# Kernel optimization log

Hardware: AMD Instinct MI355X
Metric: run time of the kernel (lower is better)

The kernel has to match this reference:

```python
import jax, jax.numpy as jnp
import numpy as np

NOISE_EPS = 0.01
TOP_K = 2


def setup_inputs() -> dict:
    key = jax.random.key(0)
    k1, k2, k3, k4 = jax.random.split(key, 4)
    B, S, D, E = 8, 4096, 1024, 16
    x = jax.random.normal(k1, (B, S, D), dtype=jnp.float32)
    noise = jax.random.normal(k2, (B * S, E), dtype=jnp.float32)
    # xavier_uniform for Linear(D, E): bound = sqrt(6/(D+E))
    bound = float(np.sqrt(6.0 / (D + E)))
    W_gate = jax.random.uniform(k3, (E, D), dtype=jnp.float32, minval=-bound, maxval=bound)
    W_noise = jax.random.uniform(k4, (E, D), dtype=jnp.float32, minval=-bound, maxval=bound)
    return {"x": x, "noise": noise, "W_gate": W_gate, "W_noise": W_noise}


def reference(x, noise, W_gate, W_noise):
    # flatten tokens: (B,S,D) -> (N,D)
    orig_shape = x.shape
    x_flat = x.reshape(-1, x.shape[-1])
    clean_logits = jnp.einsum('nd,ed->ne', x_flat, W_gate)          # (N, E)
    noise_logits = jnp.einsum('nd,ed->ne', x_flat, W_noise)         # (N, E)
    noisy_logits = clean_logits + noise * jax.nn.softplus(noise_logits) * NOISE_EPS
    gates = jax.nn.softmax(noisy_logits, axis=-1)                   # (N, E)
    top_k_gates, top_k_indices = jax.lax.top_k(gates, TOP_K)        # (N, k)
    top_k_gates = top_k_gates / (jnp.sum(top_k_gates, axis=-1, keepdims=True) + 1e-8)
    load = jnp.sum(gates, axis=0)                                    # (E,)
    new_shape = orig_shape[:-1] + (TOP_K,)
    top_k_gates = top_k_gates.reshape(new_shape)
    top_k_indices = top_k_indices.reshape(new_shape)
    return top_k_gates, top_k_indices, load
```

## Files before the change

kernel.cpp:

```cpp
#include <hip/hip_runtime.h>
#include <hip/hip_bf16.h>
#include <math.h>

#define N_TOK 32768
#define DDIM 1024
#define NEXP 16
#define THREADS 256
#define TOK_PER_WAVE 16
#define TOK_PER_BLK 64
#define NBLK (N_TOK / TOK_PER_BLK)
#define KSTEPS (DDIM / 32)

typedef __attribute__((ext_vector_type(8))) short bf16x8;
typedef __attribute__((ext_vector_type(4))) float f32x4;

__device__ inline short f2bf(float f) {
    unsigned u = __builtin_bit_cast(unsigned, f);
    u += 0x7fffu + ((u >> 16) & 1u);
    return (short)(u >> 16);
}

__global__ __launch_bounds__(256) void make_wfrag(
    const float* __restrict__ Wg, const float* __restrict__ Wn,
    unsigned short* __restrict__ Wfrag)
{
    const int i    = blockIdx.x * 256 + threadIdx.x;
    const int j    = i & 7;
    const int lane = (i >> 3) & 63;
    const int tile = (i >> 9) & 1;
    const int s    = i >> 10;
    const int k    = s * 32 + (lane >> 4) * 8 + j;
    const float* W = tile ? Wn : Wg;
    Wfrag[i] = (unsigned short)f2bf(W[(size_t)(lane & 15) * DDIM + k]);
}

__global__ __launch_bounds__(THREADS) void router_mfma(
    const float* __restrict__ x, const float* __restrict__ noise,
    const unsigned short* __restrict__ Wfrag,
    float* __restrict__ out_gates, float* __restrict__ out_idx,
    float* __restrict__ partials)
{
    __shared__ float blk_load[NEXP];
    const int tid  = threadIdx.x;
    const int lane = tid & 63;
    const int w    = tid >> 6;
    if (tid < NEXP) blk_load[tid] = 0.0f;
    __syncthreads();

    const int tok = blockIdx.x * TOK_PER_BLK + w * TOK_PER_WAVE + (lane & 15);
    const int grp = lane >> 4;

    const float*          xb = x + (size_t)tok * DDIM + grp * 8;
    const unsigned short* wb = Wfrag + (size_t)lane * 8;

    f32x4 acc0 = {0.f, 0.f, 0.f, 0.f};
    f32x4 acc1 = {0.f, 0.f, 0.f, 0.f};

#pragma unroll 4
    for (int s = 0; s < KSTEPS; ++s) {
        const float4 lo = *(const float4*)(xb + s * 32);
        const float4 hi = *(const float4*)(xb + s * 32 + 4);
        const bf16x8 a0 = *(const bf16x8*)(wb + (size_t)(s * 2 + 0) * 512);
        const bf16x8 a1 = *(const bf16x8*)(wb + (size_t)(s * 2 + 1) * 512);
        bf16x8 b;
        b[0] = f2bf(lo.x); b[1] = f2bf(lo.y); b[2] = f2bf(lo.z); b[3] = f2bf(lo.w);
        b[4] = f2bf(hi.x); b[5] = f2bf(hi.y); b[6] = f2bf(hi.z); b[7] = f2bf(hi.w);
        acc0 = __builtin_amdgcn_mfma_f32_16x16x32_bf16(a0, b, acc0, 0, 0, 0);
        acc1 = __builtin_amdgcn_mfma_f32_16x16x32_bf16(a1, b, acc1, 0, 0, 0);
    }

    const float4 nz4 = *(const float4*)(noise + (size_t)tok * NEXP + grp * 4);
    const float nzv[4] = {nz4.x, nz4.y, nz4.z, nz4.w};

    float lg[4];
#pragma unroll
    for (int r = 0; r < 4; ++r) {
        const float cl = acc0[r];
        const float nl = acc1[r];
        const float sp = fmaxf(nl, 0.0f) + log1pf(expf(-fabsf(nl)));
        lg[r] = cl + nzv[r] * sp * 0.01f;
    }

    float m = fmaxf(fmaxf(lg[0], lg[1]), fmaxf(lg[2], lg[3]));
    m = fmaxf(m, __shfl_xor(m, 16, 64));
    m = fmaxf(m, __shfl_xor(m, 32, 64));

    float p[4];
    float ssum = 0.0f;
#pragma unroll
    for (int r = 0; r < 4; ++r) { p[r] = expf(lg[r] - m); ssum += p[r]; }
    ssum += __shfl_xor(ssum, 16, 64);
    ssum += __shfl_xor(ssum, 32, 64);
    const float inv = 1.0f / ssum;

    float g[4];
#pragma unroll
    for (int r = 0; r < 4; ++r) g[r] = p[r] * inv;

    float v1 = -1.0f, v2 = -1.0f;
    int   i1 = 0,     i2 = 0;
#pragma unroll
    for (int r = 0; r < 4; ++r) {
        const float ge = g[r];
        const int   e  = grp * 4 + r;
        if (ge > v1)      { v2 = v1; i2 = i1; v1 = ge; i1 = e; }
        else if (ge > v2) { v2 = ge; i2 = e; }
    }
#pragma unroll
    for (int off = 16; off <= 32; off <<= 1) {
        const float ov1 = __shfl_xor(v1, off, 64);
        const float ov2 = __shfl_xor(v2, off, 64);
        const int   oi1 = __shfl_xor(i1, off, 64);
        const int   oi2 = __shfl_xor(i2, off, 64);
        const bool aWins = (v1 > ov1) || (v1 == ov1 && i1 < oi1);
        float nv1, nv2; int ni1, ni2;
        if (aWins) {
            nv1 = v1; ni1 = i1;
            const bool bNext = (ov1 > v2) || (ov1 == v2 && oi1 < i2);
            nv2 = bNext ? ov1 : v2;  ni2 = bNext ? oi1 : i2;
        } else {
            nv1 = ov1; ni1 = oi1;
            const bool aNext = (v1 > ov2) || (v1 == ov2 && i1 < oi2);
            nv2 = aNext ? v1 : ov2;  ni2 = aNext ? i1 : oi2;
        }
        v1 = nv1; v2 = nv2; i1 = ni1; i2 = ni2;
    }
    if (grp == 0) {
        const float den = v1 + v2 + 1e-8f;
        out_gates[(size_t)tok * 2 + 0] = v1 / den;
        out_gates[(size_t)tok * 2 + 1] = v2 / den;
        out_idx[(size_t)tok * 2 + 0] = (float)i1;
        out_idx[(size_t)tok * 2 + 1] = (float)i2;
    }

#pragma unroll
    for (int r = 0; r < 4; ++r) {
        float v = g[r];
        v += __shfl_xor(v, 1, 64);
        v += __shfl_xor(v, 2, 64);
        v += __shfl_xor(v, 4, 64);
        v += __shfl_xor(v, 8, 64);
        if ((lane & 15) == 0) atomicAdd(&blk_load[grp * 4 + r], v);
    }
    __syncthreads();
    if (tid < NEXP) partials[(size_t)blockIdx.x * NEXP + tid] = blk_load[tid];
}

__global__ __launch_bounds__(64) void reduce_load(
    const float* __restrict__ partials, float* __restrict__ out_load)
{
    const int lane = threadIdx.x;
    float loc[16];
#pragma unroll
    for (int e = 0; e < 16; ++e) loc[e] = 0.0f;
    for (int b = lane; b < NBLK; b += 64) {
        const float4* p = (const float4*)(partials + (size_t)b * 16);
#pragma unroll
        for (int j = 0; j < 4; ++j) {
            const float4 v = p[j];
            loc[j * 4 + 0] += v.x; loc[j * 4 + 1] += v.y;
            loc[j * 4 + 2] += v.z; loc[j * 4 + 3] += v.w;
        }
    }
#pragma unroll
    for (int e = 0; e < 16; ++e) {
        float v = loc[e];
#pragma unroll
        for (int off = 32; off; off >>= 1) v += __shfl_xor(v, off, 64);
        if (lane == 0) out_load[e] = v;
    }
}

extern "C" void kernel_launch(void* const* d_in, const int* in_sizes, int n_in,
                              void* d_out, int out_size, void* d_ws, size_t ws_size,
                              hipStream_t stream) {
    (void)in_sizes; (void)n_in; (void)ws_size; (void)out_size;
    const float* x     = (const float*)d_in[0];
    const float* noise = (const float*)d_in[1];
    const float* Wg    = (const float*)d_in[2];
    const float* Wn    = (const float*)d_in[3];

    float* out       = (float*)d_out;
    float* out_gates = out;
    float* out_idx   = out + (size_t)N_TOK * 2;
    float* out_load  = out + (size_t)N_TOK * 4;

    unsigned short* Wfrag = (unsigned short*)d_ws;
    float* partials = (float*)((char*)d_ws + 65536);

    make_wfrag<<<128, 256, 0, stream>>>(Wg, Wn, Wfrag);
    router_mfma<<<NBLK, THREADS, 0, stream>>>(
        x, noise, Wfrag, out_gates, out_idx, partials);
    reduce_load<<<1, 64, 0, stream>>>(partials, out_load);
}
```

Measured before the change: 40.82 us.

## Fuse weight prep and load reduction into router kernel with LDS weights and prefetch

Removes the separate weight-fragment kernel: each block converts W_gate/W_noise to bf16 fragments in 64KB of LDS. The K loop is restructured into double-buffered windows that prefetch x into registers before consuming the previous window. The final load reduction moves into the main kernel, done by whichever block finishes last (detected with an atomic counter), replacing the extra reduce launch with a memset. The cost is that every block redoes the weight conversion, LDS use rises, and the large register buffers limit occupancy.

```diff
diff --git a/kernel.cpp b/kernel.cpp
--- a/kernel.cpp
+++ b/kernel.cpp
@@ -20,54 +20,76 @@
     return (short)(u >> 16);
 }
 
-__global__ __launch_bounds__(256) void make_wfrag(
+__global__ __launch_bounds__(THREADS, 2) void router_mfma(
+    const float* __restrict__ x, const float* __restrict__ noise,
     const float* __restrict__ Wg, const float* __restrict__ Wn,
-    unsigned short* __restrict__ Wfrag)
+    float* __restrict__ out_gates, float* __restrict__ out_idx,
+    float* __restrict__ partials, int* __restrict__ counter,
+    float* __restrict__ out_load)
 {
-    const int i    = blockIdx.x * 256 + threadIdx.x;
-    const int j    = i & 7;
-    const int lane = (i >> 3) & 63;
-    const int tile = (i >> 9) & 1;
-    const int s    = i >> 10;
-    const int k    = s * 32 + (lane >> 4) * 8 + j;
-    const float* W = tile ? Wn : Wg;
-    Wfrag[i] = (unsigned short)f2bf(W[(size_t)(lane & 15) * DDIM + k]);
-}
-
-__global__ __launch_bounds__(THREADS) void router_mfma(
-    const float* __restrict__ x, const float* __restrict__ noise,
-    const unsigned short* __restrict__ Wfrag,
-    float* __restrict__ out_gates, float* __restrict__ out_idx,
-    float* __restrict__ partials)
-{
+    __shared__ unsigned short wlds[32768];
     __shared__ float blk_load[NEXP];
+    __shared__ int isLast;
+
     const int tid  = threadIdx.x;
     const int lane = tid & 63;
-    const int w    = tid >> 6;
+
+#pragma unroll
+    for (int cc = 0; cc < 16; ++cc) {
+        const int slot  = cc * 256 + tid;
+        const int laneP = slot & 63;
+        const int tile  = (slot >> 6) & 1;
+        const int s     = slot >> 7;
+        const int m     = laneP & 15;
+        const int half  = laneP >> 4;
+        const int k0    = s * 32 + half * 8;
+        const float* Wsrc = (tile ? Wn : Wg) + (size_t)m * DDIM + k0;
+        const float4 f0 = *(const float4*)Wsrc;
+        const float4 f1 = *(const float4*)(Wsrc + 4);
+        bf16x8 v;
+        v[0] = f2bf(f0.x); v[1] = f2bf(f0.y); v[2] = f2bf(f0.z); v[3] = f2bf(f0.w);
+        v[4] = f2bf(f1.x); v[5] = f2bf(f1.y); v[6] = f2bf(f1.z); v[7] = f2bf(f1.w);
+        *(bf16x8*)&wlds[(size_t)slot * 8] = v;
+    }
     if (tid < NEXP) blk_load[tid] = 0.0f;
     __syncthreads();
 
+    const int w   = tid >> 6;
     const int tok = blockIdx.x * TOK_PER_BLK + w * TOK_PER_WAVE + (lane & 15);
     const int grp = lane >> 4;
 
-    const float*          xb = x + (size_t)tok * DDIM + grp * 8;
-    const unsigned short* wb = Wfrag + (size_t)lane * 8;
+    const float* xb = x + (size_t)tok * DDIM + grp * 8;
 
     f32x4 acc0 = {0.f, 0.f, 0.f, 0.f};
     f32x4 acc1 = {0.f, 0.f, 0.f, 0.f};
 
-#pragma unroll 4
-    for (int s = 0; s < KSTEPS; ++s) {
-        const float4 lo = *(const float4*)(xb + s * 32);
-        const float4 hi = *(const float4*)(xb + s * 32 + 4);
-        const bf16x8 a0 = *(const bf16x8*)(wb + (size_t)(s * 2 + 0) * 512);
-        const bf16x8 a1 = *(const bf16x8*)(wb + (size_t)(s * 2 + 1) * 512);
-        bf16x8 b;
-        b[0] = f2bf(lo.x); b[1] = f2bf(lo.y); b[2] = f2bf(lo.z); b[3] = f2bf(lo.w);
-        b[4] = f2bf(hi.x); b[5] = f2bf(hi.y); b[6] = f2bf(hi.z); b[7] = f2bf(hi.w);
-        acc0 = __builtin_amdgcn_mfma_f32_16x16x32_bf16(a0, b, acc0, 0, 0, 0);
-        acc1 = __builtin_amdgcn_mfma_f32_16x16x32_bf16(a1, b, acc1, 0, 0, 0);
-    }
+#define LOAD_WIN(BUF, WI) do { _Pragma("unroll") \
+    for (int i = 0; i < 8; ++i) { \
+        BUF[2*i]   = *(const float4*)(xb + ((WI)*8 + i) * 32); \
+        BUF[2*i+1] = *(const float4*)(xb + ((WI)*8 + i) * 32 + 4); \
+    } } while (0)
+
+#define CONS_WIN(BUF, WI) do { _Pragma("unroll") \
+    for (int i = 0; i < 8; ++i) { \
+        const int s_ = (WI)*8 + i; \
+        const bf16x8 a0 = *(const bf16x8*)&wlds[(size_t)(s_*2 + 0) * 512 + lane * 8]; \
+        const bf16x8 a1 = *(const bf16x8*)&wlds[(size_t)(s_*2 + 1) * 512 + lane * 8]; \
+        bf16x8 b; \
+        b[0] = f2bf(BUF[2*i].x);   b[1] = f2bf(BUF[2*i].y); \
+        b[2] = f2bf(BUF[2*i].z);   b[3] = f2bf(BUF[2*i].w); \
+        b[4] = f2bf(BUF[2*i+1].x); b[5] = f2bf(BUF[2*i+1].y); \
+        b[6] = f2bf(BUF[2*i+1].z); b[7] = f2bf(BUF[2*i+1].w); \
+        acc0 = __builtin_amdgcn_mfma_f32_16x16x32_bf16(a0, b, acc0, 0, 0, 0); \
+        acc1 = __builtin_amdgcn_mfma_f32_16x16x32_bf16(a1, b, acc1, 0, 0, 0); \
+    } } while (0)
+
+    float4 XA[16], XB[16];
+    LOAD_WIN(XA, 0);
+    LOAD_WIN(XB, 1);
+    CONS_WIN(XA, 0);  LOAD_WIN(XA, 2);
+    CONS_WIN(XB, 1);  LOAD_WIN(XB, 3);
+    CONS_WIN(XA, 2);
+    CONS_WIN(XB, 3);
 
     const float4 nz4 = *(const float4*)(noise + (size_t)tok * NEXP + grp * 4);
     const float nzv[4] = {nz4.x, nz4.y, nz4.z, nz4.w};
@@ -144,31 +166,40 @@
     }
     __syncthreads();
     if (tid < NEXP) partials[(size_t)blockIdx.x * NEXP + tid] = blk_load[tid];
-}
-
-__global__ __launch_bounds__(64) void reduce_load(
-    const float* __restrict__ partials, float* __restrict__ out_load)
-{
-    const int lane = threadIdx.x;
-    float loc[16];
-#pragma unroll
-    for (int e = 0; e < 16; ++e) loc[e] = 0.0f;
-    for (int b = lane; b < NBLK; b += 64) {
-        const float4* p = (const float4*)(partials + (size_t)b * 16);
-#pragma unroll
-        for (int j = 0; j < 4; ++j) {
-            const float4 v = p[j];
-            loc[j * 4 + 0] += v.x; loc[j * 4 + 1] += v.y;
-            loc[j * 4 + 2] += v.z; loc[j * 4 + 3] += v.w;
+
+    __threadfence();
+    __syncthreads();
+    if (tid == 0) {
+        const int old = atomicAdd(counter, 1);
+        isLast = (old == NBLK - 1);
+    }
+    __syncthreads();
+    if (isLast) {
+        __threadfence();
+        if (tid < 64) {
+            float loc[16];
+#pragma unroll
+            for (int e = 0; e < 16; ++e) loc[e] = 0.0f;
+            for (int b = tid; b < NBLK; b += 64) {
+                const float4* pp = (const float4*)(partials + (size_t)b * 16);
+#pragma unroll
+                for (int j = 0; j < 4; ++j) {
+                    const float4 v = pp[j];
+                    loc[j * 4 + 0] += v.x; loc[j * 4 + 1] += v.y;
+                    loc[j * 4 + 2] += v.z; loc[j * 4 + 3] += v.w;
+                }
+            }
+#pragma unroll
+            for (int e = 0; e < 16; ++e) {
+                float v = loc[e];
+#pragma unroll
+                for (int off = 32; off; off >>= 1) v += __shfl_xor(v, off, 64);
+                if (tid == 0) out_load[e] = v;
+            }
         }
     }
-#pragma unroll
-    for (int e = 0; e < 16; ++e) {
-        float v = loc[e];
-#pragma unroll
-        for (int off = 32; off; off >>= 1) v += __shfl_xor(v, off, 64);
-        if (lane == 0) out_load[e] = v;
-    }
+#undef LOAD_WIN
+#undef CONS_WIN
 }
 
 extern "C" void kernel_launch(void* const* d_in, const int* in_sizes, int n_in,
@@ -185,11 +216,10 @@
     float* out_idx   = out + (size_t)N_TOK * 2;
     float* out_load  = out + (size_t)N_TOK * 4;
 
-    unsigned short* Wfrag = (unsigned short*)d_ws;
-    float* partials = (float*)((char*)d_ws + 65536);
-
-    make_wfrag<<<128, 256, 0, stream>>>(Wg, Wn, Wfrag);
+    int*   counter  = (int*)d_ws;
+    float* partials = (float*)((char*)d_ws + 64);
+
+    hipMemsetAsync(d_ws, 0, 64, stream);
     router_mfma<<<NBLK, THREADS, 0, stream>>>(
-        x, noise, Wfrag, out_gates, out_idx, partials);
-    reduce_load<<<1, 64, 0, stream>>>(partials, out_load);
+        x, noise, Wg, Wn, out_gates, out_idx, partials, counter, out_load);
 }
```

New measurement: 73.67 us. +80.5%, slower.

## Split K across waves and fuse load reduction via last-block counter

Applied to the files above, without the earlier changes.

Each block now handles 32 tokens, with two waves per 16-token group. Each wave covers half of the D dimension, and the two partial accumulators are combined through LDS before the softmax and top-k epilogue. This doubles the block count and the memory parallelism in flight per token. The separate reduce_load launch is removed: an atomic counter, reset in make_wfrag, lets the last block sum the per-block partials, which saves a kernel launch. In exchange it adds an LDS exchange, extra barriers, threadfence and atomic overhead, and leaves half the waves idle during the epilogue.

```diff
diff --git a/kernel.cpp b/kernel.cpp
--- a/kernel.cpp
+++ b/kernel.cpp
@@ -6,10 +6,9 @@
 #define DDIM 1024
 #define NEXP 16
 #define THREADS 256
-#define TOK_PER_WAVE 16
-#define TOK_PER_BLK 64
+#define TOK_PER_BLK 32
 #define NBLK (N_TOK / TOK_PER_BLK)
-#define KSTEPS (DDIM / 32)
+#define KH 16
 
 typedef __attribute__((ext_vector_type(8))) short bf16x8;
 typedef __attribute__((ext_vector_type(4))) float f32x4;
@@ -22,8 +21,9 @@
 
 __global__ __launch_bounds__(256) void make_wfrag(
     const float* __restrict__ Wg, const float* __restrict__ Wn,
-    unsigned short* __restrict__ Wfrag)
+    unsigned short* __restrict__ Wfrag, int* __restrict__ counter)
 {
+    if (blockIdx.x == 0 && threadIdx.x == 0) *counter = 0;
     const int i    = blockIdx.x * 256 + threadIdx.x;
     const int j    = i & 7;
     const int lane = (i >> 3) & 63;
@@ -38,26 +38,31 @@
     const float* __restrict__ x, const float* __restrict__ noise,
     const unsigned short* __restrict__ Wfrag,
     float* __restrict__ out_gates, float* __restrict__ out_idx,
-    float* __restrict__ partials)
+    float* __restrict__ partials, int* __restrict__ counter,
+    float* __restrict__ out_load)
 {
+    __shared__ float plds[2][64][8];
     __shared__ float blk_load[NEXP];
+    __shared__ int isLast;
+
     const int tid  = threadIdx.x;
     const int lane = tid & 63;
     const int w    = tid >> 6;
+    const int tg   = w >> 1;
+    const int kh   = w & 1;
     if (tid < NEXP) blk_load[tid] = 0.0f;
-    __syncthreads();
-
-    const int tok = blockIdx.x * TOK_PER_BLK + w * TOK_PER_WAVE + (lane & 15);
+
+    const int tok = blockIdx.x * TOK_PER_BLK + tg * 16 + (lane & 15);
     const int grp = lane >> 4;
 
-    const float*          xb = x + (size_t)tok * DDIM + grp * 8;
-    const unsigned short* wb = Wfrag + (size_t)lane * 8;
+    const float*          xb = x + (size_t)tok * DDIM + kh * (KH * 32) + grp * 8;
+    const unsigned short* wb = Wfrag + (size_t)lane * 8 + (size_t)kh * (KH * 2) * 512;
 
     f32x4 acc0 = {0.f, 0.f, 0.f, 0.f};
     f32x4 acc1 = {0.f, 0.f, 0.f, 0.f};
 
 #pragma unroll 4
-    for (int s = 0; s < KSTEPS; ++s) {
+    for (int s = 0; s < KH; ++s) {
         const float4 lo = *(const float4*)(xb + s * 32);
         const float4 hi = *(const float4*)(xb + s * 32 + 4);
         const bf16x8 a0 = *(const bf16x8*)(wb + (size_t)(s * 2 + 0) * 512);
@@ -69,105 +74,129 @@
         acc1 = __builtin_amdgcn_mfma_f32_16x16x32_bf16(a1, b, acc1, 0, 0, 0);
     }
 
-    const float4 nz4 = *(const float4*)(noise + (size_t)tok * NEXP + grp * 4);
-    const float nzv[4] = {nz4.x, nz4.y, nz4.z, nz4.w};
-
-    float lg[4];
-#pragma unroll
-    for (int r = 0; r < 4; ++r) {
-        const float cl = acc0[r];
-        const float nl = acc1[r];
-        const float sp = fmaxf(nl, 0.0f) + log1pf(expf(-fabsf(nl)));
-        lg[r] = cl + nzv[r] * sp * 0.01f;
-    }
-
-    float m = fmaxf(fmaxf(lg[0], lg[1]), fmaxf(lg[2], lg[3]));
-    m = fmaxf(m, __shfl_xor(m, 16, 64));
-    m = fmaxf(m, __shfl_xor(m, 32, 64));
-
-    float p[4];
-    float ssum = 0.0f;
-#pragma unroll
-    for (int r = 0; r < 4; ++r) { p[r] = expf(lg[r] - m); ssum += p[r]; }
-    ssum += __shfl_xor(ssum, 16, 64);
-    ssum += __shfl_xor(ssum, 32, 64);
-    const float inv = 1.0f / ssum;
-
-    float g[4];
-#pragma unroll
-    for (int r = 0; r < 4; ++r) g[r] = p[r] * inv;
-
-    float v1 = -1.0f, v2 = -1.0f;
-    int   i1 = 0,     i2 = 0;
-#pragma unroll
-    for (int r = 0; r < 4; ++r) {
-        const float ge = g[r];
-        const int   e  = grp * 4 + r;
-        if (ge > v1)      { v2 = v1; i2 = i1; v1 = ge; i1 = e; }
-        else if (ge > v2) { v2 = ge; i2 = e; }
-    }
-#pragma unroll
-    for (int off = 16; off <= 32; off <<= 1) {
-        const float ov1 = __shfl_xor(v1, off, 64);
-        const float ov2 = __shfl_xor(v2, off, 64);
-        const int   oi1 = __shfl_xor(i1, off, 64);
-        const int   oi2 = __shfl_xor(i2, off, 64);
-        const bool aWins = (v1 > ov1) || (v1 == ov1 && i1 < oi1);
-        float nv1, nv2; int ni1, ni2;
-        if (aWins) {
-            nv1 = v1; ni1 = i1;
-            const bool bNext = (ov1 > v2) || (ov1 == v2 && oi1 < i2);
-            nv2 = bNext ? ov1 : v2;  ni2 = bNext ? oi1 : i2;
-        } else {
-            nv1 = ov1; ni1 = oi1;
-            const bool aNext = (v1 > ov2) || (v1 == ov2 && i1 < oi2);
-            nv2 = aNext ? v1 : ov2;  ni2 = aNext ? i1 : oi2;
-        }
-        v1 = nv1; v2 = nv2; i1 = ni1; i2 = ni2;
-    }
-    if (grp == 0) {
-        const float den = v1 + v2 + 1e-8f;
-        out_gates[(size_t)tok * 2 + 0] = v1 / den;
-        out_gates[(size_t)tok * 2 + 1] = v2 / den;
-        out_idx[(size_t)tok * 2 + 0] = (float)i1;
-        out_idx[(size_t)tok * 2 + 1] = (float)i2;
-    }
-
-#pragma unroll
-    for (int r = 0; r < 4; ++r) {
-        float v = g[r];
-        v += __shfl_xor(v, 1, 64);
-        v += __shfl_xor(v, 2, 64);
-        v += __shfl_xor(v, 4, 64);
-        v += __shfl_xor(v, 8, 64);
-        if ((lane & 15) == 0) atomicAdd(&blk_load[grp * 4 + r], v);
+    if (kh == 1) {
+#pragma unroll
+        for (int r = 0; r < 4; ++r) {
+            plds[tg][lane][r]     = acc0[r];
+            plds[tg][lane][4 + r] = acc1[r];
+        }
+    }
+    __syncthreads();
+
+    if (kh == 0) {
+#pragma unroll
+        for (int r = 0; r < 4; ++r) {
+            acc0[r] += plds[tg][lane][r];
+            acc1[r] += plds[tg][lane][4 + r];
+        }
+
+        const float4 nz4 = *(const float4*)(noise + (size_t)tok * NEXP + grp * 4);
+        const float nzv[4] = {nz4.x, nz4.y, nz4.z, nz4.w};
+
+        float lg[4];
+#pragma unroll
+        for (int r = 0; r < 4; ++r) {
+            const float cl = acc0[r];
+            const float nl = acc1[r];
+            const float sp = fmaxf(nl, 0.0f) + log1pf(expf(-fabsf(nl)));
+            lg[r] = cl + nzv[r] * sp * 0.01f;
+        }
+
+        float m = fmaxf(fmaxf(lg[0], lg[1]), fmaxf(lg[2], lg[3]));
+        m = fmaxf(m, __shfl_xor(m, 16, 64));
+        m = fmaxf(m, __shfl_xor(m, 32, 64));
+
+        float p[4];
+        float ssum = 0.0f;
+#pragma unroll
+        for (int r = 0; r < 4; ++r) { p[r] = expf(lg[r] - m); ssum += p[r]; }
+        ssum += __shfl_xor(ssum, 16, 64);
+        ssum += __shfl_xor(ssum, 32, 64);
+        const float inv = 1.0f / ssum;
+
+        float g[4];
+#pragma unroll
+        for (int r = 0; r < 4; ++r) g[r] = p[r] * inv;
+
+        float v1 = -1.0f, v2 = -1.0f;
+        int   i1 = 0,     i2 = 0;
+#pragma unroll
+        for (int r = 0; r < 4; ++r) {
+            const float ge = g[r];
+            const int   e  = grp * 4 + r;
+            if (ge > v1)      { v2 = v1; i2 = i1; v1 = ge; i1 = e; }
+            else if (ge > v2) { v2 = ge; i2 = e; }
+        }
+#pragma unroll
+        for (int off = 16; off <= 32; off <<= 1) {
+            const float ov1 = __shfl_xor(v1, off, 64);
+            const float ov2 = __shfl_xor(v2, off, 64);
+            const int   oi1 = __shfl_xor(i1, off, 64);
+            const int   oi2 = __shfl_xor(i2, off, 64);
+            const bool aWins = (v1 > ov1) || (v1 == ov1 && i1 < oi1);
+            float nv1, nv2; int ni1, ni2;
+            if (aWins) {
+                nv1 = v1; ni1 = i1;
+                const bool bNext = (ov1 > v2) || (ov1 == v2 && oi1 < i2);
+                nv2 = bNext ? ov1 : v2;  ni2 = bNext ? oi1 : i2;
+            } else {
+                nv1 = ov1; ni1 = oi1;
+                const bool aNext = (v1 > ov2) || (v1 == ov2 && i1 < oi2);
+                nv2 = aNext ? v1 : ov2;  ni2 = aNext ? i1 : oi2;
+            }
+            v1 = nv1; v2 = nv2; i1 = ni1; i2 = ni2;
+        }
+        if (grp == 0) {
+            const float den = v1 + v2 + 1e-8f;
+            out_gates[(size_t)tok * 2 + 0] = v1 / den;
+            out_gates[(size_t)tok * 2 + 1] = v2 / den;
+            out_idx[(size_t)tok * 2 + 0] = (float)i1;
+            out_idx[(size_t)tok * 2 + 1] = (float)i2;
+        }
+
+#pragma unroll
+        for (int r = 0; r < 4; ++r) {
+            float v = g[r];
+            v += __shfl_xor(v, 1, 64);
+            v += __shfl_xor(v, 2, 64);
+            v += __shfl_xor(v, 4, 64);
+            v += __shfl_xor(v, 8, 64);
+            if ((lane & 15) == 0) atomicAdd(&blk_load[grp * 4 + r], v);
+        }
     }
     __syncthreads();
     if (tid < NEXP) partials[(size_t)blockIdx.x * NEXP + tid] = blk_load[tid];
-}
-
-__global__ __launch_bounds__(64) void reduce_load(
-    const float* __restrict__ partials, float* __restrict__ out_load)
-{
-    const int lane = threadIdx.x;
-    float loc[16];
-#pragma unroll
-    for (int e = 0; e < 16; ++e) loc[e] = 0.0f;
-    for (int b = lane; b < NBLK; b += 64) {
-        const float4* p = (const float4*)(partials + (size_t)b * 16);
-#pragma unroll
-        for (int j = 0; j < 4; ++j) {
-            const float4 v = p[j];
-            loc[j * 4 + 0] += v.x; loc[j * 4 + 1] += v.y;
-            loc[j * 4 + 2] += v.z; loc[j * 4 + 3] += v.w;
-        }
-    }
-#pragma unroll
-    for (int e = 0; e < 16; ++e) {
-        float v = loc[e];
-#pragma unroll
-        for (int off = 32; off; off >>= 1) v += __shfl_xor(v, off, 64);
-        if (lane == 0) out_load[e] = v;
+
+    __threadfence();
+    __syncthreads();
+    if (tid == 0) {
+        const int old = atomicAdd(counter, 1);
+        isLast = (old == NBLK - 1);
+    }
+    __syncthreads();
+    if (isLast) {
+        __threadfence();
+        if (tid < 64) {
+            float loc[16];
+#pragma unroll
+            for (int e = 0; e < 16; ++e) loc[e] = 0.0f;
+            for (int b = tid; b < NBLK; b += 64) {
+                const float4* pp = (const float4*)(partials + (size_t)b * 16);
+#pragma unroll
+                for (int j = 0; j < 4; ++j) {
+                    const float4 v = pp[j];
+                    loc[j * 4 + 0] += v.x; loc[j * 4 + 1] += v.y;
+                    loc[j * 4 + 2] += v.z; loc[j * 4 + 3] += v.w;
+                }
+            }
+#pragma unroll
+            for (int e = 0; e < 16; ++e) {
+                float v = loc[e];
+#pragma unroll
+                for (int off = 32; off; off >>= 1) v += __shfl_xor(v, off, 64);
+                if (tid == 0) out_load[e] = v;
+            }
+        }
     }
 }
 
@@ -185,11 +214,11 @@
     float* out_idx   = out + (size_t)N_TOK * 2;
     float* out_load  = out + (size_t)N_TOK * 4;
 
-    unsigned short* Wfrag = (unsigned short*)d_ws;
-    float* partials = (float*)((char*)d_ws + 65536);
-
-    make_wfrag<<<128, 256, 0, stream>>>(Wg, Wn, Wfrag);
+    int*            counter  = (int*)d_ws;
+    float*          partials = (float*)((char*)d_ws + 64);
+    unsigned short* Wfrag    = (unsigned short*)((char*)d_ws + 65536 + 64);
+
+    make_wfrag<<<128, 256, 0, stream>>>(Wg, Wn, Wfrag, counter);
     router_mfma<<<NBLK, THREADS, 0, stream>>>(
-        x, noise, Wfrag, out_gates, out_idx, partials);
-    reduce_load<<<1, 64, 0, stream>>>(partials, out_load);
-}
+        x, noise, Wfrag, out_gates, out_idx, partials, counter, out_load);
+}
```

Measured after the change: 132.9 us. 3.26x slower.
